# Kernel tuning notes

Hardware: AMD Instinct MI355X
Metric: run time of the kernel (lower is better)

Reference implementation:

```python
import jax, jax.numpy as jnp
import numpy as np

KSIZE = 11

def conv3(x, w, b):
    # 3x3 SAME conv, NCHW / OIHW
    y = jax.lax.conv_general_dilated(x, w, window_strides=(1, 1), padding='SAME',
                                     dimension_numbers=('NCHW', 'OIHW', 'NCHW'))
    return y + b[None, :, None, None]

def apply_separable_filters(rgb, kh, kv, kernel_size):
    # rgb: [B,3,H,W]; kh, kv: [B,K,H,W] (softmaxed per-pixel kernels)
    b, c, h, w = rgb.shape
    pad = kernel_size // 2
    # horizontal pass: replicate-pad width, weighted sum over K shifted slices
    xh = jnp.pad(rgb, ((0, 0), (0, 0), (0, 0), (pad, pad)), mode='edge')
    out_h = jnp.zeros_like(rgb)
    for k in range(kernel_size):
        out_h = out_h + xh[:, :, :, k:k + w] * kh[:, None, k, :, :]
    # vertical pass: replicate-pad height
    xv = jnp.pad(out_h, ((0, 0), (0, 0), (pad, pad), (0, 0)), mode='edge')
    out_v = jnp.zeros_like(rgb)
    for k in range(kernel_size):
        out_v = out_v + xv[:, :, k:k + h, :] * kv[:, None, k, :, :]
    return out_v

def get_depth_mask(depth, threshold=0.2, sharpness=15.0):
    return jax.nn.sigmoid((depth - threshold) * sharpness)

def setup_inputs() -> dict:
    key = jax.random.key(0)
    ks = jax.random.split(key, 16)
    B, H, W = 4, 512, 512
    rgb = jax.random.uniform(ks[0], (B, 3, H, W), dtype=jnp.float32)
    depth = jax.random.uniform(ks[1], (B, 1, H, W), dtype=jnp.float32)

    def cw(k, o, i):
        return jax.random.normal(k, (o, i, 3, 3), dtype=jnp.float32) * (1.0 / np.sqrt(i * 9.0))

    w1, b1 = cw(ks[2], 64, 4), jnp.zeros((64,), jnp.float32)
    w2, b2 = cw(ks[3], 64, 64), jnp.zeros((64,), jnp.float32)
    w3, b3 = cw(ks[4], 128, 64), jnp.zeros((128,), jnp.float32)
    w4, b4 = cw(ks[5], 128, 128), jnp.zeros((128,), jnp.float32)
    w5, b5 = cw(ks[6], 64, 128), jnp.zeros((64,), jnp.float32)
    wh, bh = cw(ks[7], KSIZE, 64), jnp.zeros((KSIZE,), jnp.float32)
    wv, bv = cw(ks[8], KSIZE, 64), jnp.zeros((KSIZE,), jnp.float32)
    return {"rgb": rgb, "depth": depth,
            "w1": w1, "b1": b1, "w2": w2, "b2": b2, "w3": w3, "b3": b3,
            "w4": w4, "b4": b4, "w5": w5, "b5": b5,
            "wh": wh, "bh": bh, "wv": wv, "bv": bv}

def reference(rgb, depth, w1, b1, w2, b2, w3, b3, w4, b4, w5, b5, wh, bh, wv, bv):
    focus_threshold = 0.2
    x = jnp.concatenate([rgb, depth], axis=1)  # [B,4,H,W]
    f = jax.nn.relu(conv3(x, w1, b1))
    f = jax.nn.relu(conv3(f, w2, b2))
    f = jax.nn.relu(conv3(f, w3, b3))
    f = jax.nn.relu(conv3(f, w4, b4))
    f = jax.nn.relu(conv3(f, w5, b5))
    kh = jax.nn.softmax(conv3(f, wh, bh), axis=1)  # [B,K,H,W]
    kv = jax.nn.softmax(conv3(f, wv, bv), axis=1)
    blurred = apply_separable_filters(rgb, kh, kv, KSIZE)
    mask = get_depth_mask(depth, threshold=focus_threshold)
    return mask * rgb + (1.0 - mask) * blurred
```

## Files before the change

kernel.cpp:

```cpp
#include <hip/hip_runtime.h>
#include <hip/hip_bf16.h>

using bf16 = __hip_bfloat16;
typedef short bf16x8 __attribute__((ext_vector_type(8)));
typedef float f32x4  __attribute__((ext_vector_type(4)));

static constexpr int Bn = 4, Hn = 512, Wn = 512;
static constexpr int HWn = Hn * Wn;
static constexpr int Hp = 514, Wp = 514;
static constexpr int QN = Hp * Wp;
static constexpr int QN8 = QN * 8;
static constexpr int Kn = 11, PADk = 5;

__device__ __forceinline__ float b2f(bf16 v) { return __bfloat162float(v); }
__device__ __forceinline__ bf16  f2b(float v) { return __float2bfloat16(v); }


__global__ __launch_bounds__(256) void zero_halo(bf16* __restrict__ buf, int nplanes)
{
    constexpr int PER = 2 * Wp + 2 * Hn;
    int i = blockIdx.x * 256 + threadIdx.x;
    if (i >= nplanes * PER) return;
    int p = i / PER, r = i - p * PER;
    int q;
    if (r < Wp)            q = r;
    else if (r < 2 * Wp)   q = (Hp - 1) * Wp + (r - Wp);
    else if (r < 2 * Wp + Hn) q = (r - 2 * Wp + 1) * Wp;
    else                   q = (r - 2 * Wp - Hn + 1) * Wp + (Wp - 1);
    *(uint4*)(buf + (size_t)p * QN8 + (size_t)q * 8) = uint4{0u, 0u, 0u, 0u};
}

__global__ __launch_bounds__(256) void pack8(
    const float* __restrict__ rgb, const float* __restrict__ depth,
    bf16* __restrict__ xin)
{
    int q = blockIdx.x * 256 + threadIdx.x;
    if (q >= QN) return;
    int yy = q / Wp, xx = q - yy * Wp;
    float r = 0.f, g = 0.f, b = 0.f, d = 0.f;
    if (yy >= 1 && yy <= Hn && xx >= 1 && xx <= Wn) {
        int px = (yy - 1) * Wn + (xx - 1);
        r = rgb[px]; g = rgb[HWn + px]; b = rgb[2 * HWn + px]; d = depth[px];
    }
    auto pk = [](float a, float c) {
        return (unsigned)__builtin_bit_cast(unsigned short, __float2bfloat16(a)) |
               ((unsigned)__builtin_bit_cast(unsigned short, __float2bfloat16(c)) << 16);
    };
    uint4 o; o.x = pk(r, g); o.y = pk(b, d); o.z = 0u; o.w = 0u;
    *(uint4*)(xin + (size_t)q * 8) = o;
}

__global__ void prep_wtF(const float* __restrict__ w, bf16* __restrict__ dst,
                         int COUT, int CIN, int CINP, int TAPSP)
{
    int K = CINP * TAPSP, NCB = COUT / 16;
    int idx = blockIdx.x * 256 + threadIdx.x;
    if (idx >= COUT * K) return;
    int j = idx & 7, lane = (idx >> 3) & 63;
    int rest = idx >> 9;
    int c16b = rest % NCB, ks = rest / NCB;
    int co = c16b * 16 + (lane & 15);
    int k  = ks * 32 + (lane >> 4) * 8 + j;
    int tap = k / CINP, ci = k - tap * CINP;
    float v = (tap < 9 && ci < CIN) ? w[((size_t)co * CIN + ci) * 9 + tap] : 0.f;
    dst[idx] = f2b(v);
}

__global__ void prep_hvF(const float* __restrict__ wh, const float* __restrict__ wv,
                         bf16* __restrict__ dst)
{
    int idx = blockIdx.x * 256 + threadIdx.x;
    if (idx >= 32 * 576) return;
    int j = idx & 7, lane = (idx >> 3) & 63;
    int rest = idx >> 9;
    int c16b = rest & 1, ks = rest >> 1;
    int co = c16b * 16 + (lane & 15);
    int k  = ks * 32 + (lane >> 4) * 8 + j;
    int tap = k / 64, ci = k & 63;
    float v = 0.f;
    if (tap < 9) {
        if (co < 11)      v = wh[((size_t)co * 64 + ci) * 9 + tap];
        else if (co < 22) v = wv[((size_t)(co - 11) * 64 + ci) * 9 + tap];
    }
    dst[idx] = f2b(v);
}

__global__ void prep_bias_hv(const float* __restrict__ bh, const float* __restrict__ bv,
                             float* __restrict__ dst)
{
    int i = threadIdx.x;
    if (i < 32) dst[i] = (i < 11) ? bh[i] : ((i < 22) ? bv[i - 11] : 0.f);
}

template<int CINP, int COUT, int TAPSP, int NFM, bool RELU, bool OUTF32>
__global__ __launch_bounds__(256, 2) void conv_gemm(
    const bf16* __restrict__ in, const bf16* __restrict__ wtF,
    const float* __restrict__ bias, void* __restrict__ outv)
{
    constexpr int K    = CINP * TAPSP;
    constexpr int NK   = K / 32;
    constexpr int NCB  = COUT / 16;
    constexpr int NFN  = NCB;
    constexpr int BM   = 4 * NFM * 16;
    constexpr int GX   = 512 / BM;
    constexpr int OSZ  = OUTF32 ? 4 : 2;
    constexpr int TILEB = BM * COUT * OSZ;
    constexpr int PCB  = BM * 8 * OSZ;

    __shared__ char smem[TILEB];

    const int tid  = threadIdx.x;
    const int lane = tid & 63, wid = tid >> 6;
    const int l15  = lane & 15, l4 = lane >> 4;

    const int nwg  = GX * 512;
    int orig = (int)blockIdx.y * GX + (int)blockIdx.x;
    int sbid = (orig & 7) * (nwg >> 3) + (orig >> 3);
    const int bx = (GX == 1) ? 0 : (sbid & (GX - 1));
    const int by = (GX == 1) ? sbid : (sbid / GX);

    const int qblk = (by + 1) * Wp + 1 + bx * BM;
    const int q0   = qblk + wid * (NFM * 16);

    int abase[NFM];
#pragma unroll
    for (int mf = 0; mf < NFM; ++mf) {
        int q = q0 + mf * 16 + l15;
        abase[mf] = q * 8 + ((CINP == 8) ? 0 : l4 * QN8);
    }

    auto loadA = [&](int ks, bf16x8 (&a)[NFM]) {
        if constexpr (CINP == 8) {
            int tap = ks * 4 + l4;
            int dy  = tap / 3;
            int off = (tap < 9) ? (dy - 1) * Wp + (tap - dy * 3 - 1) : 0;
#pragma unroll
            for (int mf = 0; mf < NFM; ++mf)
                a[mf] = *(const bf16x8*)(in + abase[mf] + off * 8);
        } else {
            const int kk  = ks * 32;
            const int tap = kk / CINP;
            const int cib = kk - tap * CINP;
            const int pb  = cib >> 3;
            const int dy  = tap / 3;
            const int off = (dy - 1) * Wp + (tap - dy * 3 - 1);
            const int stp = pb * QN8 + off * 8;
#pragma unroll
            for (int mf = 0; mf < NFM; ++mf)
                a[mf] = *(const bf16x8*)(in + abase[mf] + stp);
        }
    };
    auto loadB = [&](int ks, bf16x8 (&bfr)[NFN]) {
        const bf16* bp = wtF + lane * 8;
#pragma unroll
        for (int nf = 0; nf < NFN; ++nf)
            bfr[nf] = *(const bf16x8*)(bp + (ks * NCB + nf) * 512);
    };

    f32x4 acc[NFM][NFN];
#pragma unroll
    for (int mf = 0; mf < NFM; ++mf)
#pragma unroll
        for (int nf = 0; nf < NFN; ++nf) acc[mf][nf] = f32x4{0.f, 0.f, 0.f, 0.f};

    auto step = [&](bf16x8 (&a)[NFM], bf16x8 (&bfr)[NFN]) {
#pragma unroll
        for (int mf = 0; mf < NFM; ++mf)
#pragma unroll
            for (int nf = 0; nf < NFN; ++nf)
                acc[mf][nf] = __builtin_amdgcn_mfma_f32_16x16x32_bf16(
                    a[mf], bfr[nf], acc[mf][nf], 0, 0, 0);
    };

    bf16x8 a0[NFM], a1[NFM], b0[NFN], b1[NFN];
    loadA(0, a0); loadB(0, b0);
    for (int ks = 0; ks + 1 < NK; ks += 2) {
        loadA(ks + 1, a1); loadB(ks + 1, b1);
        step(a0, b0);
        if (ks + 2 < NK) { loadA(ks + 2, a0); loadB(ks + 2, b0); }
        step(a1, b1);
    }
    if constexpr (NK & 1) step(a0, b0);

#pragma unroll
    for (int nf = 0; nf < NFN; ++nf) {
        const int co = nf * 16 + l15;
        const float bv = bias[co];
#pragma unroll
        for (int mf = 0; mf < NFM; ++mf) {
#pragma unroll
            for (int r = 0; r < 4; ++r) {
                float v = acc[mf][nf][r] + bv;
                if constexpr (RELU) v = fmaxf(v, 0.f);
                const int pl = wid * (NFM * 16) + mf * 16 + l4 * 4 + r;
                const int eo = ((co >> 3) * BM + pl) * 8 + (co & 7);
                if constexpr (OUTF32)
                    ((float*)smem)[eo] = v;
                else
                    ((bf16*)smem)[eo] = f2b(v);
            }
        }
    }
    __syncthreads();
    char* gbase = (char*)outv;
    for (int ofs = tid * 16; ofs < TILEB; ofs += 4096) {
        const int p = ofs / PCB, w = ofs - p * PCB;
        char* dst = gbase + ((size_t)p * QN8 + (size_t)qblk * 8) * OSZ + w;
        *(uint4*)dst = *(const uint4*)(smem + ofs);
    }
}

__global__ __launch_bounds__(256) void softmax_hv(
    const float* __restrict__ logits, float* __restrict__ khI, float* __restrict__ kvI)
{
    int px = blockIdx.x * 256 + threadIdx.x;
    int y = px >> 9, x = px & (Wn - 1);
    int q = (y + 1) * Wp + x + 1;
    float c[32];
#pragma unroll
    for (int p = 0; p < 4; ++p) {
        const float* L = logits + (size_t)p * QN8 + (size_t)q * 8;
#pragma unroll
        for (int j = 0; j < 8; ++j) c[p * 8 + j] = L[j];
    }
    float h[Kn], v[Kn];
#pragma unroll
    for (int k = 0; k < Kn; ++k) { h[k] = c[k]; v[k] = c[11 + k]; }

    float mh = h[0], mv = v[0];
#pragma unroll
    for (int k = 1; k < Kn; ++k) { mh = fmaxf(mh, h[k]); mv = fmaxf(mv, v[k]); }
    float sh = 0.f, sv = 0.f;
#pragma unroll
    for (int k = 0; k < Kn; ++k) {
        h[k] = __expf(h[k] - mh); sh += h[k];
        v[k] = __expf(v[k] - mv); sv += v[k];
    }
    const float ih = 1.f / sh, iv = 1.f / sv;
    float* oh = khI + (size_t)px * 12;
    float* ov = kvI + (size_t)px * 12;
#pragma unroll
    for (int k = 0; k < Kn; ++k) { oh[k] = h[k] * ih; ov[k] = v[k] * iv; }
    oh[11] = 0.f; ov[11] = 0.f;
}

__global__ __launch_bounds__(256) void hblur(
    const float* __restrict__ rgb, const float* __restrict__ khI,
    float* __restrict__ outh)
{
    const int px = blockIdx.x * 256 + threadIdx.x;
    const int y = px >> 9, x = px & (Wn - 1);
    const float* kp = khI + (size_t)px * 12;
    float kk[Kn];
#pragma unroll
    for (int k = 0; k < Kn; ++k) kk[k] = kp[k];

#pragma unroll
    for (int c = 0; c < 3; ++c) {
        const float* r = rgb + (size_t)c * HWn + (size_t)y * Wn;
        float s = 0.f;
#pragma unroll
        for (int k = 0; k < Kn; ++k) {
            int xx = x + k - PADk;
            xx = min(max(xx, 0), Wn - 1);
            s += r[xx] * kk[k];
        }
        outh[(size_t)c * HWn + px] = s;
    }
}

__global__ __launch_bounds__(256) void vblur_compose(
    const float* __restrict__ outh, const float* __restrict__ kvI,
    const float* __restrict__ rgb, const float* __restrict__ depth,
    float* __restrict__ out)
{
    const int px = blockIdx.x * 256 + threadIdx.x;
    const int y = px >> 9, x = px & (Wn - 1);
    const float* kp = kvI + (size_t)px * 12;
    float kk[Kn];
#pragma unroll
    for (int k = 0; k < Kn; ++k) kk[k] = kp[k];

    const float d = depth[px];
    const float m = 1.f / (1.f + __expf(-(d - 0.2f) * 15.f));

#pragma unroll
    for (int c = 0; c < 3; ++c) {
        const float* col = outh + (size_t)c * HWn + x;
        float s = 0.f;
#pragma unroll
        for (int k = 0; k < Kn; ++k) {
            int yy = y + k - PADk;
            yy = min(max(yy, 0), Hn - 1);
            s += col[(size_t)yy * Wn] * kk[k];
        }
        const float r = rgb[(size_t)c * HWn + px];
        out[(size_t)c * HWn + px] = m * r + (1.f - m) * s;
    }
}

extern "C" void kernel_launch(void* const* d_in, const int* in_sizes, int n_in,
                              void* d_out, int out_size, void* d_ws, size_t ws_size,
                              hipStream_t stream)
{
    const float* rgb   = (const float*)d_in[0];
    const float* depth = (const float*)d_in[1];
    const float* w1 = (const float*)d_in[2];  const float* b1 = (const float*)d_in[3];
    const float* w2 = (const float*)d_in[4];  const float* b2 = (const float*)d_in[5];
    const float* w3 = (const float*)d_in[6];  const float* b3 = (const float*)d_in[7];
    const float* w4 = (const float*)d_in[8];  const float* b4 = (const float*)d_in[9];
    const float* w5 = (const float*)d_in[10]; const float* b5 = (const float*)d_in[11];
    const float* wh = (const float*)d_in[12]; const float* bh = (const float*)d_in[13];
    const float* wv = (const float*)d_in[14]; const float* bv = (const float*)d_in[15];

    char* ws = (char*)d_ws;
    size_t off = 0;
    auto alloc = [&](size_t bytes) -> void* {
        void* p = ws + off;
        off += (bytes + 255) & ~(size_t)255;
        return p;
    };

    bf16*  xin  = (bf16*)alloc((size_t)QN * 8   * 2);
    bf16*  fA   = (bf16*)alloc((size_t)QN * 128 * 2);
    bf16*  fB   = (bf16*)alloc((size_t)QN * 128 * 2);
    float* khI  = (float*)alloc((size_t)HWn * 12 * 4);
    float* kvI  = (float*)alloc((size_t)HWn * 12 * 4);
    float* oh   = (float*)alloc((size_t)HWn * 3  * 4);
    bf16*  wt1  = (bf16*)alloc(64  * 96   * 2);
    bf16*  wt2  = (bf16*)alloc(64  * 576  * 2);
    bf16*  wt3  = (bf16*)alloc(128 * 576  * 2);
    bf16*  wt4  = (bf16*)alloc(128 * 1152 * 2);
    bf16*  wt5  = (bf16*)alloc(64  * 1152 * 2);
    bf16*  wtHV = (bf16*)alloc(32  * 576  * 2);
    float* bHV  = (float*)alloc(32 * 4);
    float* logits = (float*)fB;
    (void)ws_size;

    prep_wtF<<<(64 * 96   + 255) / 256, 256, 0, stream>>>(w1, wt1, 64, 4,   8,   12);
    prep_wtF<<<(64 * 576  + 255) / 256, 256, 0, stream>>>(w2, wt2, 64, 64,  64,  9);
    prep_wtF<<<(128* 576  + 255) / 256, 256, 0, stream>>>(w3, wt3, 128, 64, 64,  9);
    prep_wtF<<<(128* 1152 + 255) / 256, 256, 0, stream>>>(w4, wt4, 128, 128, 128, 9);
    prep_wtF<<<(64 * 1152 + 255) / 256, 256, 0, stream>>>(w5, wt5, 64, 128, 128, 9);
    prep_hvF<<<(32 * 576  + 255) / 256, 256, 0, stream>>>(wh, wv, wtHV);
    prep_bias_hv<<<1, 32, 0, stream>>>(bh, bv, bHV);

    constexpr int HALO_THREADS = 16 * (2 * Wp + 2 * Hn);

    for (int b = 0; b < Bn; ++b) {
        const float* rgb_b   = rgb   + (size_t)b * 3 * HWn;
        const float* depth_b = depth + (size_t)b * HWn;
        float*       out_b   = (float*)d_out + (size_t)b * 3 * HWn;

        zero_halo<<<(HALO_THREADS + 255) / 256, 256, 0, stream>>>(fA, 16);
        zero_halo<<<(HALO_THREADS + 255) / 256, 256, 0, stream>>>(fB, 16);

        pack8<<<(QN + 255) / 256, 256, 0, stream>>>(rgb_b, depth_b, xin);

        conv_gemm<8,   64,  12, 4, true,  false><<<dim3(2, 512), 256, 0, stream>>>(xin, wt1, b1, fA);
        conv_gemm<64,  64,  9,  8, true,  false><<<dim3(1, 512), 256, 0, stream>>>(fA,  wt2, b2, fB);
        conv_gemm<64,  128, 9,  4, true,  false><<<dim3(2, 512), 256, 0, stream>>>(fB,  wt3, b3, fA);
        conv_gemm<128, 128, 9,  4, true,  false><<<dim3(2, 512), 256, 0, stream>>>(fA,  wt4, b4, fB);
        conv_gemm<128, 64,  9,  8, true,  false><<<dim3(1, 512), 256, 0, stream>>>(fB,  wt5, b5, fA);
        conv_gemm<64,  32,  9,  4, false, true ><<<dim3(2, 512), 256, 0, stream>>>(fA,  wtHV, bHV, logits);

        softmax_hv<<<HWn / 256, 256, 0, stream>>>(logits, khI, kvI);
        hblur<<<HWn / 256, 256, 0, stream>>>(rgb_b, khI, oh);
        vblur_compose<<<HWn / 256, 256, 0, stream>>>(oh, kvI, rgb_b, depth_b, out_b);
    }
}
```

Before: 1.281 ms.

## Split conv GEMM warps across output channels and deepen A-load pipeline

For 128-output-channel convs, the four waves now form a 2x2 grid over pixels and channel blocks, so each wave holds half the accumulators and the pixel tile per block halves. Layers 2 and 5 move to NFM=4 and launch twice as many blocks. Launch bounds rise to 3 blocks per CU, and a triple-buffered A / double-buffered B load schedule is used when NK is a multiple of 6. The fA halo zeroing is hoisted out of the batch loop. The aim is lower register pressure and more occupancy to hide latency, at the cost of more redundant A loads and smaller tiles.

```diff
diff --git a/kernel.cpp b/kernel.cpp
--- a/kernel.cpp
+++ b/kernel.cpp
@@ -93,15 +93,17 @@
 }
 
 template<int CINP, int COUT, int TAPSP, int NFM, bool RELU, bool OUTF32>
-__global__ __launch_bounds__(256, 2) void conv_gemm(
+__global__ __launch_bounds__(256, 3) void conv_gemm(
     const bf16* __restrict__ in, const bf16* __restrict__ wtF,
     const float* __restrict__ bias, void* __restrict__ outv)
 {
     constexpr int K    = CINP * TAPSP;
     constexpr int NK   = K / 32;
     constexpr int NCB  = COUT / 16;
-    constexpr int NFN  = NCB;
-    constexpr int BM   = 4 * NFM * 16;
+    constexpr int NWN  = (COUT == 128) ? 2 : 1;
+    constexpr int NWM  = 4 / NWN;
+    constexpr int NFN  = NCB / NWN;
+    constexpr int BM   = NWM * NFM * 16;
     constexpr int GX   = 512 / BM;
     constexpr int OSZ  = OUTF32 ? 4 : 2;
     constexpr int TILEB = BM * COUT * OSZ;
@@ -112,6 +114,9 @@
     const int tid  = threadIdx.x;
     const int lane = tid & 63, wid = tid >> 6;
     const int l15  = lane & 15, l4 = lane >> 4;
+    const int wmi  = (NWN == 2) ? (wid & 1) : wid;
+    const int wni  = (NWN == 2) ? (wid >> 1) : 0;
+    const int cbb  = wni * NFN;
 
     const int nwg  = GX * 512;
     int orig = (int)blockIdx.y * GX + (int)blockIdx.x;
@@ -120,7 +125,7 @@
     const int by = (GX == 1) ? sbid : (sbid / GX);
 
     const int qblk = (by + 1) * Wp + 1 + bx * BM;
-    const int q0   = qblk + wid * (NFM * 16);
+    const int q0   = qblk + wmi * (NFM * 16);
 
     int abase[NFM];
 #pragma unroll
@@ -154,7 +159,7 @@
         const bf16* bp = wtF + lane * 8;
 #pragma unroll
         for (int nf = 0; nf < NFN; ++nf)
-            bfr[nf] = *(const bf16x8*)(bp + (ks * NCB + nf) * 512);
+            bfr[nf] = *(const bf16x8*)(bp + (size_t)(ks * NCB + cbb + nf) * 512);
     };
 
     f32x4 acc[NFM][NFN];
@@ -172,19 +177,41 @@
                     a[mf], bfr[nf], acc[mf][nf], 0, 0, 0);
     };
 
-    bf16x8 a0[NFM], a1[NFM], b0[NFN], b1[NFN];
-    loadA(0, a0); loadB(0, b0);
-    for (int ks = 0; ks + 1 < NK; ks += 2) {
-        loadA(ks + 1, a1); loadB(ks + 1, b1);
-        step(a0, b0);
-        if (ks + 2 < NK) { loadA(ks + 2, a0); loadB(ks + 2, b0); }
-        step(a1, b1);
-    }
-    if constexpr (NK & 1) step(a0, b0);
+    if constexpr (NK >= 12 && NK % 6 == 0) {
+        bf16x8 a0[NFM], a1[NFM], a2[NFM], b0[NFN], b1[NFN];
+        loadA(0, a0); loadB(0, b0);
+        loadA(1, a1); loadB(1, b1);
+        loadA(2, a2);
+        int ks = 0;
+        for (; ks + 6 < NK; ks += 6) {
+            step(a0, b0); loadA(ks + 3, a0); loadB(ks + 2, b0);
+            step(a1, b1); loadA(ks + 4, a1); loadB(ks + 3, b1);
+            step(a2, b0); loadA(ks + 5, a2); loadB(ks + 4, b0);
+            step(a0, b1); loadA(ks + 6, a0); loadB(ks + 5, b1);
+            step(a1, b0); loadA(ks + 7, a1); loadB(ks + 6, b0);
+            step(a2, b1); loadA(ks + 8, a2); loadB(ks + 7, b1);
+        }
+        step(a0, b0); loadA(ks + 3, a0); loadB(ks + 2, b0);
+        step(a1, b1); loadA(ks + 4, a1); loadB(ks + 3, b1);
+        step(a2, b0); loadA(ks + 5, a2); loadB(ks + 4, b0);
+        step(a0, b1); loadB(ks + 5, b1);
+        step(a1, b0);
+        step(a2, b1);
+    } else {
+        bf16x8 a0[NFM], a1[NFM], b0[NFN], b1[NFN];
+        loadA(0, a0); loadB(0, b0);
+        for (int ks = 0; ks + 1 < NK; ks += 2) {
+            loadA(ks + 1, a1); loadB(ks + 1, b1);
+            step(a0, b0);
+            if (ks + 2 < NK) { loadA(ks + 2, a0); loadB(ks + 2, b0); }
+            step(a1, b1);
+        }
+        if constexpr (NK & 1) step(a0, b0);
+    }
 
 #pragma unroll
     for (int nf = 0; nf < NFN; ++nf) {
-        const int co = nf * 16 + l15;
+        const int co = (cbb + nf) * 16 + l15;
         const float bv = bias[co];
 #pragma unroll
         for (int mf = 0; mf < NFM; ++mf) {
@@ -192,7 +219,7 @@
             for (int r = 0; r < 4; ++r) {
                 float v = acc[mf][nf][r] + bv;
                 if constexpr (RELU) v = fmaxf(v, 0.f);
-                const int pl = wid * (NFM * 16) + mf * 16 + l4 * 4 + r;
+                const int pl = wmi * (NFM * 16) + mf * 16 + l4 * 4 + r;
                 const int eo = ((co >> 3) * BM + pl) * 8 + (co & 7);
                 if constexpr (OUTF32)
                     ((float*)smem)[eo] = v;
@@ -347,21 +374,22 @@
 
     constexpr int HALO_THREADS = 16 * (2 * Wp + 2 * Hn);
 
+    zero_halo<<<(HALO_THREADS + 255) / 256, 256, 0, stream>>>(fA, 16);
+
     for (int b = 0; b < Bn; ++b) {
         const float* rgb_b   = rgb   + (size_t)b * 3 * HWn;
         const float* depth_b = depth + (size_t)b * HWn;
         float*       out_b   = (float*)d_out + (size_t)b * 3 * HWn;
 
-        zero_halo<<<(HALO_THREADS + 255) / 256, 256, 0, stream>>>(fA, 16);
         zero_halo<<<(HALO_THREADS + 255) / 256, 256, 0, stream>>>(fB, 16);
 
         pack8<<<(QN + 255) / 256, 256, 0, stream>>>(rgb_b, depth_b, xin);
 
         conv_gemm<8,   64,  12, 4, true,  false><<<dim3(2, 512), 256, 0, stream>>>(xin, wt1, b1, fA);
-        conv_gemm<64,  64,  9,  8, true,  false><<<dim3(1, 512), 256, 0, stream>>>(fA,  wt2, b2, fB);
-        conv_gemm<64,  128, 9,  4, true,  false><<<dim3(2, 512), 256, 0, stream>>>(fB,  wt3, b3, fA);
-        conv_gemm<128, 128, 9,  4, true,  false><<<dim3(2, 512), 256, 0, stream>>>(fA,  wt4, b4, fB);
-        conv_gemm<128, 64,  9,  8, true,  false><<<dim3(1, 512), 256, 0, stream>>>(fB,  wt5, b5, fA);
+        conv_gemm<64,  64,  9,  4, true,  false><<<dim3(2, 512), 256, 0, stream>>>(fA,  wt2, b2, fB);
+        conv_gemm<64,  128, 9,  4, true,  false><<<dim3(4, 512), 256, 0, stream>>>(fB,  wt3, b3, fA);
+        conv_gemm<128, 128, 9,  4, true,  false><<<dim3(4, 512), 256, 0, stream>>>(fA,  wt4, b4, fB);
+        conv_gemm<128, 64,  9,  4, true,  false><<<dim3(2, 512), 256, 0, stream>>>(fB,  wt5, b5, fA);
         conv_gemm<64,  32,  9,  4, false, true ><<<dim3(2, 512), 256, 0, stream>>>(fA,  wtHV, bHV, logits);
 
         softmax_hv<<<HWn / 256, 256, 0, stream>>>(logits, khI, kvI);
```

Result: slower. 1.837 ms (+43.4%).

## Retile conv GEMM into 2D pixel tiles with warp split over output channels

Applied to the files above, without the earlier changes.

Replaces the 1D row-strip tiling of the implicit-GEMM conv with 2D tiles of 64 pixels by up to 4 rows. For 128-output-channel layers the waves are split 2x2 across rows and channel halves, which cuts per-wave accumulator registers and allows occupancy 3 in launch bounds. Overlapping 3x3 neighbourhoods across rows in a block are meant to improve cache reuse. The fA halo zeroing is hoisted out of the batch loop. Risks include more blocks with smaller tiles, more redundant weight loads per block, and the store epilogue now writing several row segments per block.

```diff
diff --git a/kernel.cpp b/kernel.cpp
--- a/kernel.cpp
+++ b/kernel.cpp
@@ -92,35 +92,43 @@
     if (i < 32) dst[i] = (i < 11) ? bh[i] : ((i < 22) ? bv[i - 11] : 0.f);
 }
 
-template<int CINP, int COUT, int TAPSP, int NFM, bool RELU, bool OUTF32>
-__global__ __launch_bounds__(256, 2) void conv_gemm(
+template<int CINP, int COUT, int TAPSP, bool RELU, bool OUTF32>
+__global__ __launch_bounds__(256, 3) void conv_gemm(
     const bf16* __restrict__ in, const bf16* __restrict__ wtF,
     const float* __restrict__ bias, void* __restrict__ outv)
 {
     constexpr int K    = CINP * TAPSP;
     constexpr int NK   = K / 32;
     constexpr int NCB  = COUT / 16;
-    constexpr int NFN  = NCB;
-    constexpr int BM   = 4 * NFM * 16;
-    constexpr int GX   = 512 / BM;
+    constexpr int NWN  = (COUT == 128) ? 2 : 1;
+    constexpr int NWM  = 4 / NWN;
+    constexpr int RB   = NWM;
+    constexpr int NFM  = 4;
+    constexpr int NFN  = NCB / NWN;
+    constexpr int TW   = 64;
+    constexpr int GXT  = Wn / TW;
+    constexpr int GYT  = Hn / RB;
     constexpr int OSZ  = OUTF32 ? 4 : 2;
-    constexpr int TILEB = BM * COUT * OSZ;
-    constexpr int PCB  = BM * 8 * OSZ;
+    constexpr int TILEB = RB * TW * COUT * OSZ;
+    constexpr int CHB  = TW * 8 * OSZ;
 
     __shared__ char smem[TILEB];
 
     const int tid  = threadIdx.x;
     const int lane = tid & 63, wid = tid >> 6;
     const int l15  = lane & 15, l4 = lane >> 4;
-
-    const int nwg  = GX * 512;
-    int orig = (int)blockIdx.y * GX + (int)blockIdx.x;
+    const int wmi  = (NWN == 2) ? (wid & 1) : wid;
+    const int wni  = (NWN == 2) ? (wid >> 1) : 0;
+    const int cbb  = wni * NFN;
+
+    const int nwg  = GXT * GYT;
+    int orig = (int)blockIdx.y * GXT + (int)blockIdx.x;
     int sbid = (orig & 7) * (nwg >> 3) + (orig >> 3);
-    const int bx = (GX == 1) ? 0 : (sbid & (GX - 1));
-    const int by = (GX == 1) ? sbid : (sbid / GX);
-
-    const int qblk = (by + 1) * Wp + 1 + bx * BM;
-    const int q0   = qblk + wid * (NFM * 16);
+    const int bx = sbid % GXT;
+    const int by = sbid / GXT;
+
+    const int qblk = (by * RB + 1) * Wp + 1 + bx * TW;
+    const int q0   = qblk + wmi * Wp;
 
     int abase[NFM];
 #pragma unroll
@@ -154,7 +162,7 @@
         const bf16* bp = wtF + lane * 8;
 #pragma unroll
         for (int nf = 0; nf < NFN; ++nf)
-            bfr[nf] = *(const bf16x8*)(bp + (ks * NCB + nf) * 512);
+            bfr[nf] = *(const bf16x8*)(bp + (size_t)(ks * NCB + cbb + nf) * 512);
     };
 
     f32x4 acc[NFM][NFN];
@@ -184,7 +192,7 @@
 
 #pragma unroll
     for (int nf = 0; nf < NFN; ++nf) {
-        const int co = nf * 16 + l15;
+        const int co = (cbb + nf) * 16 + l15;
         const float bv = bias[co];
 #pragma unroll
         for (int mf = 0; mf < NFM; ++mf) {
@@ -192,8 +200,8 @@
             for (int r = 0; r < 4; ++r) {
                 float v = acc[mf][nf][r] + bv;
                 if constexpr (RELU) v = fmaxf(v, 0.f);
-                const int pl = wid * (NFM * 16) + mf * 16 + l4 * 4 + r;
-                const int eo = ((co >> 3) * BM + pl) * 8 + (co & 7);
+                const int px = mf * 16 + l4 * 4 + r;
+                const int eo = (((co >> 3) * RB + wmi) * TW + px) * 8 + (co & 7);
                 if constexpr (OUTF32)
                     ((float*)smem)[eo] = v;
                 else
@@ -204,8 +212,9 @@
     __syncthreads();
     char* gbase = (char*)outv;
     for (int ofs = tid * 16; ofs < TILEB; ofs += 4096) {
-        const int p = ofs / PCB, w = ofs - p * PCB;
-        char* dst = gbase + ((size_t)p * QN8 + (size_t)qblk * 8) * OSZ + w;
+        const int c = ofs / CHB, w = ofs - c * CHB;
+        const int p = c / RB, rrow = c - p * RB;
+        char* dst = gbase + ((size_t)p * QN8 + (size_t)(qblk + rrow * Wp) * 8) * OSZ + w;
         *(uint4*)dst = *(const uint4*)(smem + ofs);
     }
 }
@@ -347,22 +356,23 @@
 
     constexpr int HALO_THREADS = 16 * (2 * Wp + 2 * Hn);
 
+    zero_halo<<<(HALO_THREADS + 255) / 256, 256, 0, stream>>>(fA, 16);
+
     for (int b = 0; b < Bn; ++b) {
         const float* rgb_b   = rgb   + (size_t)b * 3 * HWn;
         const float* depth_b = depth + (size_t)b * HWn;
         float*       out_b   = (float*)d_out + (size_t)b * 3 * HWn;
 
-        zero_halo<<<(HALO_THREADS + 255) / 256, 256, 0, stream>>>(fA, 16);
         zero_halo<<<(HALO_THREADS + 255) / 256, 256, 0, stream>>>(fB, 16);
 
         pack8<<<(QN + 255) / 256, 256, 0, stream>>>(rgb_b, depth_b, xin);
 
-        conv_gemm<8,   64,  12, 4, true,  false><<<dim3(2, 512), 256, 0, stream>>>(xin, wt1, b1, fA);
-        conv_gemm<64,  64,  9,  8, true,  false><<<dim3(1, 512), 256, 0, stream>>>(fA,  wt2, b2, fB);
-        conv_gemm<64,  128, 9,  4, true,  false><<<dim3(2, 512), 256, 0, stream>>>(fB,  wt3, b3, fA);
-        conv_gemm<128, 128, 9,  4, true,  false><<<dim3(2, 512), 256, 0, stream>>>(fA,  wt4, b4, fB);
-        conv_gemm<128, 64,  9,  8, true,  false><<<dim3(1, 512), 256, 0, stream>>>(fB,  wt5, b5, fA);
-        conv_gemm<64,  32,  9,  4, false, true ><<<dim3(2, 512), 256, 0, stream>>>(fA,  wtHV, bHV, logits);
+        conv_gemm<8,   64,  12, true,  false><<<dim3(8, 128), 256, 0, stream>>>(xin, wt1, b1, fA);
+        conv_gemm<64,  64,  9,  true,  false><<<dim3(8, 128), 256, 0, stream>>>(fA,  wt2, b2, fB);
+        conv_gemm<64,  128, 9,  true,  false><<<dim3(8, 256), 256, 0, stream>>>(fB,  wt3, b3, fA);
+        conv_gemm<128, 128, 9,  true,  false><<<dim3(8, 256), 256, 0, stream>>>(fA,  wt4, b4, fB);
+        conv_gemm<128, 64,  9,  true,  false><<<dim3(8, 128), 256, 0, stream>>>(fB,  wt5, b5, fA);
+        conv_gemm<64,  32,  9,  false, true ><<<dim3(8, 128), 256, 0, stream>>>(fA,  wtHV, bHV, logits);
 
         softmax_hv<<<HWn / 256, 256, 0, stream>>>(logits, khI, kvI);
         hblur<<<HWn / 256, 256, 0, stream>>>(rgb_b, khI, oh);
```

New measurement: 1.446 ms. 12.9% more time.
